# Kernel optimization log

Measured on AMD Instinct MI355X. Metric: run time of the kernel, lower is better.

Reference implementation:

```python
import jax, jax.numpy as jnp
import numpy as np

N_NODES = 50000
N_EDGES = 600000
D = 128
NEG_SLOPE = (1.0 / 8.0 + 1.0 / 3.0) / 2.0  # RReLU in eval mode: mean of (lower, upper)


def setup_inputs() -> dict:
    key = jax.random.key(0)
    ks = jax.random.split(key, 16)
    inp = {
        'node_feats': jax.random.normal(ks[0], (N_NODES, D), dtype=jnp.float32),
        'edge_feats': jax.random.normal(ks[1], (N_EDGES, D), dtype=jnp.float32),
        'src': jax.random.randint(ks[2], (N_EDGES,), 0, N_NODES, dtype=jnp.int32),
        'dst': jax.random.randint(ks[3], (N_EDGES,), 0, N_NODES, dtype=jnp.int32),
    }
    scale = 1.0 / np.sqrt(D)
    i = 4
    for l in range(2):
        for w in (1, 2, 3):
            inp[f'W{w}_l{l}'] = jax.random.uniform(ks[i], (D, D), jnp.float32, -scale, scale); i += 1
            inp[f'b{w}_l{l}'] = jnp.zeros((D,), jnp.float32)
    return inp


def _layer(h, efeat, src, dst, W1, b1, W2, b2, W3, b3):
    # per-edge message: linear1(src_h + edge_h)  [E, D]
    m = (h[src] + efeat) @ W1 + b1
    # attention score per edge: <h_dst, m_e>
    score = jnp.sum(h[dst] * m, axis=-1)  # [E]
    smax = jax.ops.segment_max(score, dst, num_segments=N_NODES)
    smax = jnp.where(jnp.isfinite(smax), smax, 0.0)
    w = jnp.exp(score - smax[dst])  # [E]
    denom = jax.ops.segment_sum(w, dst, num_segments=N_NODES)  # [N]
    wsum = jax.ops.segment_sum(w[:, None] * m, dst, num_segments=N_NODES)  # [N, D]
    neigh = wsum / jnp.maximum(denom, 1e-30)[:, None]
    deg = jax.ops.segment_sum(jnp.ones_like(score), dst, num_segments=N_NODES)
    self_msg = h @ W2 + b2
    iso_msg = h @ W3 + b3
    self_msg = jnp.where((deg == 0)[:, None], iso_msg, self_msg)
    x = self_msg + neigh
    return jnp.where(x >= 0, x, x * NEG_SLOPE)


def reference(node_feats, edge_feats, src, dst,
              W1_l0, b1_l0, W2_l0, b2_l0, W3_l0, b3_l0,
              W1_l1, b1_l1, W2_l1, b2_l1, W3_l1, b3_l1):
    h = _layer(node_feats, edge_feats, src, dst, W1_l0, b1_l0, W2_l0, b2_l0, W3_l0, b3_l0)
    h = _layer(h, edge_feats, src, dst, W1_l1, b1_l1, W2_l1, b2_l1, W3_l1, b3_l1)
    return h
```

## Files before the change

kernel.cpp:

```cpp
#include <hip/hip_runtime.h>


typedef unsigned short u16;
typedef short bf16x8 __attribute__((ext_vector_type(8)));
typedef float f32x4 __attribute__((ext_vector_type(4)));

#define NEG_SLOPE 0.22916666666666666f

__device__ inline float bf2f(u16 h) { return __uint_as_float(((unsigned)h) << 16); }
__device__ inline u16 f2bf(float f) {
  unsigned u = __float_as_uint(f);
  u += 0x7fffu + ((u >> 16) & 1u);
  return (u16)(u >> 16);
}

__global__ __launch_bounds__(256)
void prep_weights(const float* w0, const float* w1, const float* w2,
                  const float* w3, const float* w4, const float* w5,
                  const float* c0, const float* c1, const float* c2,
                  const float* c3, const float* c4, const float* c5,
                  u16* __restrict__ wf, float* __restrict__ bf) {
  int b = blockIdx.x, tid = threadIdx.x;
  const float* Ws[8] = {w0, w1, w2, w3, w4, w5, w0, w3};
  const float* Cs[6] = {c0, c1, c2, c3, c4, c5};
  const float* W = Ws[b];
  const bool tr = (b >= 6);
  u16* out = wf + (size_t)b * 32768;
  for (int q = 0; q < 64; ++q) {
    int fi = tid * 64 + q;
    int t = fi >> 11, kc = (fi >> 9) & 3, lane = (fi >> 3) & 63, j = fi & 7;
    int k = kc * 32 + (lane >> 4) * 8 + j;
    int n = t * 16 + (lane & 15);
    float w = tr ? W[n * 128 + k] : W[k * 128 + n];
    u16 hi = f2bf(w);
    u16 lo = f2bf(w - bf2f(hi));
    int base = ((t * 4 + kc) * 2) * 512 + lane * 8 + j;
    out[base] = hi;
    out[base + 512] = lo;
  }
  if (b < 6 && tid < 128) bf[b * 128 + tid] = Cs[b][tid];
}

__global__ __launch_bounds__(256)
void hist_k(const int* __restrict__ dst, int* __restrict__ deg, int E) {
  int i = blockIdx.x * 256 + threadIdx.x;
  int stride = gridDim.x * 256;
  for (; i < E; i += stride) atomicAdd(&deg[dst[i]], 1);
}

__global__ __launch_bounds__(256)
void scan1(const int* __restrict__ deg, int* __restrict__ off,
           int* __restrict__ bsum, int N) {
  __shared__ int sh[256];
  int b = blockIdx.x, t = threadIdx.x;
  int base = b * 1024 + t * 4;
  int v[4];
  #pragma unroll
  for (int i = 0; i < 4; ++i) v[i] = (base + i < N) ? deg[base + i] : 0;
  int s = v[0] + v[1] + v[2] + v[3];
  sh[t] = s;
  __syncthreads();
  for (int o = 1; o < 256; o <<= 1) {
    int x = (t >= o) ? sh[t - o] : 0;
    __syncthreads();
    sh[t] += x;
    __syncthreads();
  }
  int run = sh[t] - s;
  #pragma unroll
  for (int i = 0; i < 4; ++i) {
    if (base + i < N) off[base + i] = run;
    run += v[i];
  }
  if (t == 255) bsum[b] = sh[255];
}

__global__ void scan2(int* __restrict__ bsum, int nb) {
  __shared__ int sh[256];
  int t = threadIdx.x;
  int v = (t < nb) ? bsum[t] : 0;
  sh[t] = v;
  __syncthreads();
  for (int o = 1; o < 256; o <<= 1) {
    int x = (t >= o) ? sh[t - o] : 0;
    __syncthreads();
    sh[t] += x;
    __syncthreads();
  }
  if (t < nb) bsum[t] = sh[t] - v;
}

__global__ __launch_bounds__(256)
void scan3(int* __restrict__ off, const int* __restrict__ bsum,
           int* __restrict__ cursor, int N, int E) {
  int i = blockIdx.x * 256 + threadIdx.x;
  if (i < N) {
    int v = off[i] + bsum[i >> 10];
    off[i] = v;
    cursor[i] = v;
  } else if (i == N) {
    off[N] = E;
  }
}

__global__ __launch_bounds__(256)
void scatter_k(const int* __restrict__ dst, const int* __restrict__ src,
               int* __restrict__ cursor, int* __restrict__ eidx,
               int* __restrict__ csrc, int E) {
  int i = blockIdx.x * 256 + threadIdx.x;
  int stride = gridDim.x * 256;
  for (; i < E; i += stride) {
    int p = atomicAdd(&cursor[dst[i]], 1);
    eidx[p] = i;
    csrc[p] = src[i];
  }
}

__global__ __launch_bounds__(256)
void gemm_n4(const float* __restrict__ A,
             const u16* __restrict__ wf1, const u16* __restrict__ wfT,
             const u16* __restrict__ wf2, const u16* __restrict__ wf3,
             const float* __restrict__ biases,
             float* __restrict__ C0, float* __restrict__ C1,
             float* __restrict__ C2, float* __restrict__ C3,
             float* __restrict__ hb1, int M) {
  __shared__ u16 ah[64 * 136];
  __shared__ u16 al[64 * 136];
  const int tid = threadIdx.x;
  const long long rowBase = (long long)blockIdx.x * 64;
  #pragma unroll
  for (int it = 0; it < 8; ++it) {
    int idx = it * 256 + tid;
    int row = idx >> 5, c4 = idx & 31;
    long long gr = rowBase + row;
    float4 v = make_float4(0.f, 0.f, 0.f, 0.f);
    if (gr < M) v = ((const float4*)A)[gr * 32 + c4];
    u16 hb[4] = {f2bf(v.x), f2bf(v.y), f2bf(v.z), f2bf(v.w)};
    u16 lb[4] = {f2bf(v.x - bf2f(hb[0])), f2bf(v.y - bf2f(hb[1])),
                 f2bf(v.z - bf2f(hb[2])), f2bf(v.w - bf2f(hb[3]))};
    *(uint2*)&ah[row * 136 + c4 * 4] = *(uint2*)hb;
    *(uint2*)&al[row * 136 + c4 * 4] = *(uint2*)lb;
  }
  __syncthreads();
  const int wid = tid >> 6, lane = tid & 63, lrow = lane & 15, lk = lane >> 4;
  bf16x8 af[4], alf[4];
  #pragma unroll
  for (int kc = 0; kc < 4; ++kc) {
    af[kc]  = *(const bf16x8*)&ah[(wid * 16 + lrow) * 136 + kc * 32 + lk * 8];
    alf[kc] = *(const bf16x8*)&al[(wid * 16 + lrow) * 136 + kc * 32 + lk * 8];
  }
  const u16* wfs[4] = {wf1, wfT, wf2, wf3};
  float* Cs[4] = {C0, C1, C2, C3};
  for (int m = 0; m < 4; ++m) {
    const u16* wf = wfs[m];
    float* C = Cs[m];
    f32x4 acc[8];
    #pragma unroll
    for (int t = 0; t < 8; ++t) acc[t] = (f32x4){0.f, 0.f, 0.f, 0.f};
    #pragma unroll
    for (int t = 0; t < 8; ++t) {
      #pragma unroll
      for (int kc = 0; kc < 4; ++kc) {
        bf16x8 bh = *(const bf16x8*)&wf[((t * 4 + kc) * 2) * 512 + lane * 8];
        bf16x8 bl = *(const bf16x8*)&wf[((t * 4 + kc) * 2 + 1) * 512 + lane * 8];
        acc[t] = __builtin_amdgcn_mfma_f32_16x16x32_bf16(af[kc],  bh, acc[t], 0, 0, 0);
        acc[t] = __builtin_amdgcn_mfma_f32_16x16x32_bf16(alf[kc], bh, acc[t], 0, 0, 0);
        acc[t] = __builtin_amdgcn_mfma_f32_16x16x32_bf16(af[kc],  bl, acc[t], 0, 0, 0);
      }
    }
    #pragma unroll
    for (int t = 0; t < 8; ++t) {
      int col = t * 16 + lrow;
      float bv = (m == 2) ? biases[128 + col] : (m == 3) ? biases[256 + col] : 0.f;
      #pragma unroll
      for (int r = 0; r < 4; ++r) {
        long long row = rowBase + wid * 16 + lk * 4 + r;
        if (row < M) C[row * 128 + col] = acc[t][r] + bv;
      }
    }
  }
  {
    int r = tid >> 2, p = tid & 3;
    long long row = rowBase + r;
    if (row < M) {
      float s = 0.f;
      #pragma unroll
      for (int k = 0; k < 32; ++k) {
        int kk = p * 32 + k;
        s += (bf2f(ah[r * 136 + kk]) + bf2f(al[r * 136 + kk])) * biases[kk];
      }
      s += __shfl_xor(s, 1);
      s += __shfl_xor(s, 2);
      if (p == 0) hb1[row] = s;
    }
  }
}

__global__ __launch_bounds__(256)
void edge_agg(const float* __restrict__ efeat, const float* __restrict__ hW1,
              const float* __restrict__ hT1, const float* __restrict__ h,
              const float* __restrict__ hb1, const int* __restrict__ off,
              const int* __restrict__ eidx, const int* __restrict__ csrc,
              float* __restrict__ X, float* __restrict__ P, int N) {
  int node = blockIdx.x * 4 + (threadIdx.x >> 6);
  if (node >= N) return;
  const int lane = threadIdx.x & 63;
  const size_t nb = (size_t)node * 128 + 2 * lane;
  int s0 = off[node], s1 = off[node + 1];
  if (s1 == s0) {
    *(float2*)&X[nb] = make_float2(0.f, 0.f);
    *(float2*)&P[nb] = make_float2(0.f, 0.f);
    return;
  }
  const float2 hn = *(const float2*)&h[nb];
  const float2 ht = *(const float2*)&hT1[nb];
  const float hb = hb1[node];
  float mx = -3.4e38f, den = 0.f;
  float aEx = 0.f, aEy = 0.f, aHx = 0.f, aHy = 0.f;
  for (int base = s0; base < s1; base += 64) {
    int cnt = s1 - base;
    if (cnt > 64) cnt = 64;
    int me = 0, ms = 0;
    if (lane < cnt) { me = eidx[base + lane]; ms = csrc[base + lane]; }
    int e0 = __shfl(me, 0), sA = __shfl(ms, 0);
    float2 ef = *(const float2*)&efeat[(size_t)e0 * 128 + 2 * lane];
    float2 hw = *(const float2*)&hW1[(size_t)sA * 128 + 2 * lane];
    for (int j = 0; j < cnt; ++j) {
      float2 efc = ef, hwc = hw;
      if (j + 1 < cnt) {
        int e1 = __shfl(me, j + 1), sB = __shfl(ms, j + 1);
        ef = *(const float2*)&efeat[(size_t)e1 * 128 + 2 * lane];
        hw = *(const float2*)&hW1[(size_t)sB * 128 + 2 * lane];
      }
      float psum = efc.x * ht.x + efc.y * ht.y + hwc.x * hn.x + hwc.y * hn.y;
      #pragma unroll
      for (int o = 32; o > 0; o >>= 1) psum += __shfl_xor(psum, o);
      float score = psum + hb;
      if (score > mx) {
        float r = __expf(mx - score);
        den *= r; aEx *= r; aEy *= r; aHx *= r; aHy *= r;
        mx = score;
      }
      float w = __expf(score - mx);
      den += w;
      aEx += w * efc.x; aEy += w * efc.y;
      aHx += w * hwc.x; aHy += w * hwc.y;
    }
  }
  float inv = 1.f / den;
  *(float2*)&X[nb] = make_float2(aEx * inv, aEy * inv);
  *(float2*)&P[nb] = make_float2(aHx * inv, aHy * inv);
}

__global__ __launch_bounds__(256)
void gemm_fin(const float* __restrict__ A,
              const u16* __restrict__ wf,
              const float* __restrict__ biases,
              const float* __restrict__ y2, const float* __restrict__ y3,
              const float* __restrict__ P, const int* __restrict__ off,
              float* __restrict__ C, int M) {
  __shared__ u16 ah[64 * 136];
  __shared__ u16 al[64 * 136];
  const int tid = threadIdx.x;
  const long long rowBase = (long long)blockIdx.x * 64;
  #pragma unroll
  for (int it = 0; it < 8; ++it) {
    int idx = it * 256 + tid;
    int row = idx >> 5, c4 = idx & 31;
    long long gr = rowBase + row;
    float4 v = make_float4(0.f, 0.f, 0.f, 0.f);
    if (gr < M) v = ((const float4*)A)[gr * 32 + c4];
    u16 hb[4] = {f2bf(v.x), f2bf(v.y), f2bf(v.z), f2bf(v.w)};
    u16 lb[4] = {f2bf(v.x - bf2f(hb[0])), f2bf(v.y - bf2f(hb[1])),
                 f2bf(v.z - bf2f(hb[2])), f2bf(v.w - bf2f(hb[3]))};
    *(uint2*)&ah[row * 136 + c4 * 4] = *(uint2*)hb;
    *(uint2*)&al[row * 136 + c4 * 4] = *(uint2*)lb;
  }
  __syncthreads();
  const int wid = tid >> 6, lane = tid & 63, lrow = lane & 15, lk = lane >> 4;
  bf16x8 af[4], alf[4];
  #pragma unroll
  for (int kc = 0; kc < 4; ++kc) {
    af[kc]  = *(const bf16x8*)&ah[(wid * 16 + lrow) * 136 + kc * 32 + lk * 8];
    alf[kc] = *(const bf16x8*)&al[(wid * 16 + lrow) * 136 + kc * 32 + lk * 8];
  }
  f32x4 acc[8];
  #pragma unroll
  for (int t = 0; t < 8; ++t) acc[t] = (f32x4){0.f, 0.f, 0.f, 0.f};
  #pragma unroll
  for (int t = 0; t < 8; ++t) {
    #pragma unroll
    for (int kc = 0; kc < 4; ++kc) {
      bf16x8 bh = *(const bf16x8*)&wf[((t * 4 + kc) * 2) * 512 + lane * 8];
      bf16x8 bl = *(const bf16x8*)&wf[((t * 4 + kc) * 2 + 1) * 512 + lane * 8];
      acc[t] = __builtin_amdgcn_mfma_f32_16x16x32_bf16(af[kc],  bh, acc[t], 0, 0, 0);
      acc[t] = __builtin_amdgcn_mfma_f32_16x16x32_bf16(alf[kc], bh, acc[t], 0, 0, 0);
      acc[t] = __builtin_amdgcn_mfma_f32_16x16x32_bf16(af[kc],  bl, acc[t], 0, 0, 0);
    }
  }
  #pragma unroll
  for (int r = 0; r < 4; ++r) {
    long long row = rowBase + wid * 16 + lk * 4 + r;
    if (row >= M) continue;
    int dg = off[row + 1] - off[row];
    #pragma unroll
    for (int t = 0; t < 8; ++t) {
      int col = t * 16 + lrow;
      size_t o = (size_t)row * 128 + col;
      float v = dg ? (acc[t][r] + y2[o] + biases[col] + P[o]) : y3[o];
      v = v >= 0.f ? v : v * NEG_SLOPE;
      C[o] = v;
    }
  }
}

extern "C" void kernel_launch(void* const* d_in, const int* in_sizes, int n_in,
                              void* d_out, int out_size, void* d_ws, size_t ws_size,
                              hipStream_t stream) {
  const int D = 128;
  const int N = in_sizes[0] / D;
  const int E = in_sizes[1] / D;

  const float* node  = (const float*)d_in[0];
  const float* edgef = (const float*)d_in[1];
  const int* src = (const int*)d_in[2];
  const int* dst = (const int*)d_in[3];

  char* p = (char*)d_ws;
  u16*   wfrag = (u16*)p;   p += (size_t)8 * 32768 * 2;
  float* biasf = (float*)p; p += 4096;
  float* hW1   = (float*)p; p += (size_t)N * 512;
  float* hT1   = (float*)p; p += (size_t)N * 512;
  float* y2    = (float*)p; p += (size_t)N * 512;
  float* y3    = (float*)p; p += (size_t)N * 512;
  float* h1    = (float*)p; p += (size_t)N * 512;
  float* Xb    = (float*)p; p += (size_t)N * 512;
  float* Pb    = (float*)p; p += (size_t)N * 512;
  float* hb1   = (float*)p; p += (size_t)N * 4;
  int* deg     = (int*)p;   p += (size_t)N * 4;
  int* off     = (int*)p;   p += (size_t)(N + 256) * 4;
  int* cursor  = (int*)p;   p += (size_t)N * 4;
  int* bsum    = (int*)p;   p += 1024;
  int* eidx    = (int*)p;   p += (size_t)E * 4;
  int* csrc    = (int*)p;   p += (size_t)E * 4;
  (void)ws_size;

  prep_weights<<<8, 256, 0, stream>>>(
      (const float*)d_in[4],  (const float*)d_in[6],  (const float*)d_in[8],
      (const float*)d_in[10], (const float*)d_in[12], (const float*)d_in[14],
      (const float*)d_in[5],  (const float*)d_in[7],  (const float*)d_in[9],
      (const float*)d_in[11], (const float*)d_in[13], (const float*)d_in[15],
      wfrag, biasf);

  const int gN = (N + 63) / 64;
  const int eB = (E + 255) / 256;
  const int nb = (N + 1023) / 1024;

  hipMemsetAsync(deg, 0, (size_t)N * 4, stream);
  hist_k<<<eB, 256, 0, stream>>>(dst, deg, E);
  scan1<<<nb, 256, 0, stream>>>(deg, off, bsum, N);
  scan2<<<1, 256, 0, stream>>>(bsum, nb);
  scan3<<<(N + 256) / 256, 256, 0, stream>>>(off, bsum, cursor, N, E);
  scatter_k<<<eB, 256, 0, stream>>>(dst, src, cursor, eidx, csrc, E);

  for (int l = 0; l < 2; ++l) {
    const float* h = (l == 0) ? node : h1;
    float* hout = (l == 0) ? h1 : (float*)d_out;
    const u16* wf1 = wfrag + (size_t)(l * 3 + 0) * 32768;
    const u16* wf2 = wfrag + (size_t)(l * 3 + 1) * 32768;
    const u16* wf3 = wfrag + (size_t)(l * 3 + 2) * 32768;
    const u16* wfT = wfrag + (size_t)(6 + l) * 32768;
    const float* bset = biasf + l * 384;

    gemm_n4<<<gN, 256, 0, stream>>>(h, wf1, wfT, wf2, wf3, bset,
                                    hW1, hT1, y2, y3, hb1, N);
    edge_agg<<<(N + 3) / 4, 256, 0, stream>>>(edgef, hW1, hT1, h, hb1,
                                              off, eidx, csrc, Xb, Pb, N);
    gemm_fin<<<gN, 256, 0, stream>>>(Xb, wf1, bset, y2, y3, Pb, off, hout, N);
  }
}
```

Before: 932.2 us.

## Aggregate raw h_src+edge features, then apply W1 once per node

Because W1 is linear, the edge kernel now accumulates the softmax-weighted sum of (h[src] + efeat) into one buffer. The final GEMM applies W1 and b1 to that aggregate, replacing the per-node hW1 projection and the separate X/P buffers. The per-dst bias term in the score is dropped, which is exact since the softmax is invariant to a per-segment shift. This removes one of the four node GEMMs, one N×128 write and read, and half the edge-loop accumulators. Separately, weight preparation is spread over 64 blocks instead of 8.

```diff
diff --git a/kernel.cpp b/kernel.cpp
--- a/kernel.cpp
+++ b/kernel.cpp
@@ -20,14 +20,16 @@
                   const float* c0, const float* c1, const float* c2,
                   const float* c3, const float* c4, const float* c5,
                   u16* __restrict__ wf, float* __restrict__ bf) {
-  int b = blockIdx.x, tid = threadIdx.x;
+  int bid = blockIdx.x, tid = threadIdx.x;
+  int b = bid >> 3, qc = (bid & 7) * 8;
   const float* Ws[8] = {w0, w1, w2, w3, w4, w5, w0, w3};
   const float* Cs[6] = {c0, c1, c2, c3, c4, c5};
   const float* W = Ws[b];
   const bool tr = (b >= 6);
   u16* out = wf + (size_t)b * 32768;
-  for (int q = 0; q < 64; ++q) {
-    int fi = tid * 64 + q;
+  #pragma unroll
+  for (int qq = 0; qq < 8; ++qq) {
+    int fi = tid * 64 + qc + qq;
     int t = fi >> 11, kc = (fi >> 9) & 3, lane = (fi >> 3) & 63, j = fi & 7;
     int k = kc * 32 + (lane >> 4) * 8 + j;
     int n = t * 16 + (lane & 15);
@@ -38,7 +40,7 @@
     out[base] = hi;
     out[base + 512] = lo;
   }
-  if (b < 6 && tid < 128) bf[b * 128 + tid] = Cs[b][tid];
+  if ((bid & 7) == 0 && b < 6 && tid < 128) bf[b * 128 + tid] = Cs[b][tid];
 }
 
 __global__ __launch_bounds__(256)
@@ -117,13 +119,11 @@
 }
 
 __global__ __launch_bounds__(256)
-void gemm_n4(const float* __restrict__ A,
-             const u16* __restrict__ wf1, const u16* __restrict__ wfT,
-             const u16* __restrict__ wf2, const u16* __restrict__ wf3,
-             const float* __restrict__ biases,
-             float* __restrict__ C0, float* __restrict__ C1,
-             float* __restrict__ C2, float* __restrict__ C3,
-             float* __restrict__ hb1, int M) {
+void gemm_n3t(const float* __restrict__ A,
+              const u16* __restrict__ wfT, const u16* __restrict__ wf2,
+              const u16* __restrict__ wf3, const float* __restrict__ biases,
+              float* __restrict__ C0, float* __restrict__ C1,
+              float* __restrict__ C2, int M) {
   __shared__ u16 ah[64 * 136];
   __shared__ u16 al[64 * 136];
   const int tid = threadIdx.x;
@@ -149,9 +149,9 @@
     af[kc]  = *(const bf16x8*)&ah[(wid * 16 + lrow) * 136 + kc * 32 + lk * 8];
     alf[kc] = *(const bf16x8*)&al[(wid * 16 + lrow) * 136 + kc * 32 + lk * 8];
   }
-  const u16* wfs[4] = {wf1, wfT, wf2, wf3};
-  float* Cs[4] = {C0, C1, C2, C3};
-  for (int m = 0; m < 4; ++m) {
+  const u16* wfs[3] = {wfT, wf2, wf3};
+  float* Cs[3] = {C0, C1, C2};
+  for (int m = 0; m < 3; ++m) {
     const u16* wf = wfs[m];
     float* C = Cs[m];
     f32x4 acc[8];
@@ -171,7 +171,7 @@
     #pragma unroll
     for (int t = 0; t < 8; ++t) {
       int col = t * 16 + lrow;
-      float bv = (m == 2) ? biases[128 + col] : (m == 3) ? biases[256 + col] : 0.f;
+      float bv = (m == 1) ? biases[128 + col] : (m == 2) ? biases[256 + col] : 0.f;
       #pragma unroll
       for (int r = 0; r < 4; ++r) {
         long long row = rowBase + wid * 16 + lk * 4 + r;
@@ -179,44 +179,24 @@
       }
     }
   }
-  {
-    int r = tid >> 2, p = tid & 3;
-    long long row = rowBase + r;
-    if (row < M) {
-      float s = 0.f;
-      #pragma unroll
-      for (int k = 0; k < 32; ++k) {
-        int kk = p * 32 + k;
-        s += (bf2f(ah[r * 136 + kk]) + bf2f(al[r * 136 + kk])) * biases[kk];
-      }
-      s += __shfl_xor(s, 1);
-      s += __shfl_xor(s, 2);
-      if (p == 0) hb1[row] = s;
-    }
-  }
-}
-
-__global__ __launch_bounds__(256)
-void edge_agg(const float* __restrict__ efeat, const float* __restrict__ hW1,
-              const float* __restrict__ hT1, const float* __restrict__ h,
-              const float* __restrict__ hb1, const int* __restrict__ off,
+}
+
+__global__ __launch_bounds__(256)
+void edge_agg(const float* __restrict__ efeat, const float* __restrict__ h,
+              const float* __restrict__ hT1, const int* __restrict__ off,
               const int* __restrict__ eidx, const int* __restrict__ csrc,
-              float* __restrict__ X, float* __restrict__ P, int N) {
+              float* __restrict__ U, int N) {
   int node = blockIdx.x * 4 + (threadIdx.x >> 6);
   if (node >= N) return;
   const int lane = threadIdx.x & 63;
   const size_t nb = (size_t)node * 128 + 2 * lane;
   int s0 = off[node], s1 = off[node + 1];
   if (s1 == s0) {
-    *(float2*)&X[nb] = make_float2(0.f, 0.f);
-    *(float2*)&P[nb] = make_float2(0.f, 0.f);
+    *(float2*)&U[nb] = make_float2(0.f, 0.f);
     return;
   }
-  const float2 hn = *(const float2*)&h[nb];
   const float2 ht = *(const float2*)&hT1[nb];
-  const float hb = hb1[node];
-  float mx = -3.4e38f, den = 0.f;
-  float aEx = 0.f, aEy = 0.f, aHx = 0.f, aHy = 0.f;
+  float mx = -3.4e38f, den = 0.f, ux = 0.f, uy = 0.f;
   for (int base = s0; base < s1; base += 64) {
     int cnt = s1 - base;
     if (cnt > 64) cnt = 64;
@@ -224,32 +204,29 @@
     if (lane < cnt) { me = eidx[base + lane]; ms = csrc[base + lane]; }
     int e0 = __shfl(me, 0), sA = __shfl(ms, 0);
     float2 ef = *(const float2*)&efeat[(size_t)e0 * 128 + 2 * lane];
-    float2 hw = *(const float2*)&hW1[(size_t)sA * 128 + 2 * lane];
+    float2 hs = *(const float2*)&h[(size_t)sA * 128 + 2 * lane];
     for (int j = 0; j < cnt; ++j) {
-      float2 efc = ef, hwc = hw;
+      float vx = ef.x + hs.x, vy = ef.y + hs.y;
       if (j + 1 < cnt) {
         int e1 = __shfl(me, j + 1), sB = __shfl(ms, j + 1);
         ef = *(const float2*)&efeat[(size_t)e1 * 128 + 2 * lane];
-        hw = *(const float2*)&hW1[(size_t)sB * 128 + 2 * lane];
+        hs = *(const float2*)&h[(size_t)sB * 128 + 2 * lane];
       }
-      float psum = efc.x * ht.x + efc.y * ht.y + hwc.x * hn.x + hwc.y * hn.y;
+      float psum = vx * ht.x + vy * ht.y;
       #pragma unroll
       for (int o = 32; o > 0; o >>= 1) psum += __shfl_xor(psum, o);
-      float score = psum + hb;
-      if (score > mx) {
-        float r = __expf(mx - score);
-        den *= r; aEx *= r; aEy *= r; aHx *= r; aHy *= r;
-        mx = score;
+      if (psum > mx) {
+        float r = __expf(mx - psum);
+        den *= r; ux *= r; uy *= r;
+        mx = psum;
       }
-      float w = __expf(score - mx);
+      float w = __expf(psum - mx);
       den += w;
-      aEx += w * efc.x; aEy += w * efc.y;
-      aHx += w * hwc.x; aHy += w * hwc.y;
+      ux += w * vx; uy += w * vy;
     }
   }
   float inv = 1.f / den;
-  *(float2*)&X[nb] = make_float2(aEx * inv, aEy * inv);
-  *(float2*)&P[nb] = make_float2(aHx * inv, aHy * inv);
+  *(float2*)&U[nb] = make_float2(ux * inv, uy * inv);
 }
 
 __global__ __launch_bounds__(256)
@@ -257,8 +234,7 @@
               const u16* __restrict__ wf,
               const float* __restrict__ biases,
               const float* __restrict__ y2, const float* __restrict__ y3,
-              const float* __restrict__ P, const int* __restrict__ off,
-              float* __restrict__ C, int M) {
+              const int* __restrict__ off, float* __restrict__ C, int M) {
   __shared__ u16 ah[64 * 136];
   __shared__ u16 al[64 * 136];
   const int tid = threadIdx.x;
@@ -307,7 +283,9 @@
     for (int t = 0; t < 8; ++t) {
       int col = t * 16 + lrow;
       size_t o = (size_t)row * 128 + col;
-      float v = dg ? (acc[t][r] + y2[o] + biases[col] + P[o]) : y3[o];
+      float v;
+      if (dg) v = acc[t][r] + y2[o] + biases[col];
+      else    v = y3[o];
       v = v >= 0.f ? v : v * NEG_SLOPE;
       C[o] = v;
     }
@@ -329,14 +307,11 @@
   char* p = (char*)d_ws;
   u16*   wfrag = (u16*)p;   p += (size_t)8 * 32768 * 2;
   float* biasf = (float*)p; p += 4096;
-  float* hW1   = (float*)p; p += (size_t)N * 512;
   float* hT1   = (float*)p; p += (size_t)N * 512;
   float* y2    = (float*)p; p += (size_t)N * 512;
   float* y3    = (float*)p; p += (size_t)N * 512;
   float* h1    = (float*)p; p += (size_t)N * 512;
-  float* Xb    = (float*)p; p += (size_t)N * 512;
-  float* Pb    = (float*)p; p += (size_t)N * 512;
-  float* hb1   = (float*)p; p += (size_t)N * 4;
+  float* Ub    = (float*)p; p += (size_t)N * 512;
   int* deg     = (int*)p;   p += (size_t)N * 4;
   int* off     = (int*)p;   p += (size_t)(N + 256) * 4;
   int* cursor  = (int*)p;   p += (size_t)N * 4;
@@ -345,7 +320,7 @@
   int* csrc    = (int*)p;   p += (size_t)E * 4;
   (void)ws_size;
 
-  prep_weights<<<8, 256, 0, stream>>>(
+  prep_weights<<<64, 256, 0, stream>>>(
       (const float*)d_in[4],  (const float*)d_in[6],  (const float*)d_in[8],
       (const float*)d_in[10], (const float*)d_in[12], (const float*)d_in[14],
       (const float*)d_in[5],  (const float*)d_in[7],  (const float*)d_in[9],
@@ -372,10 +347,9 @@
     const u16* wfT = wfrag + (size_t)(6 + l) * 32768;
     const float* bset = biasf + l * 384;
 
-    gemm_n4<<<gN, 256, 0, stream>>>(h, wf1, wfT, wf2, wf3, bset,
-                                    hW1, hT1, y2, y3, hb1, N);
-    edge_agg<<<(N + 3) / 4, 256, 0, stream>>>(edgef, hW1, hT1, h, hb1,
-                                              off, eidx, csrc, Xb, Pb, N);
-    gemm_fin<<<gN, 256, 0, stream>>>(Xb, wf1, bset, y2, y3, Pb, off, hout, N);
-  }
-}
+    gemm_n3t<<<gN, 256, 0, stream>>>(h, wfT, wf2, wf3, bset, hT1, y2, y3, N);
+    edge_agg<<<(N + 3) / 4, 256, 0, stream>>>(edgef, h, hT1, off, eidx, csrc,
+                                              Ub, N);
+    gemm_fin<<<gN, 256, 0, stream>>>(Ub, wf1, bset, y2, y3, off, hout, N);
+  }
+}
```

New measurement: 892.6 us. -4.2%, faster.
